# Optimization experiments

Measured on AMD Instinct MI355X. Metric: run time of the kernel, lower is better.

## Reference

```python
import jax, jax.numpy as jnp
import numpy as np

N_NODES = 100000
N_EDGES = 800000
IN_C = 128
HID = 256
N_GRAPHS = 64
N_CLASSES = 2
BN_EPS = 1e-5


def setup_inputs() -> dict:
    key = jax.random.key(0)
    ks = jax.random.split(key, 10)
    s1 = 1.0 / np.sqrt(IN_C)
    s2 = 1.0 / np.sqrt(HID)
    s3 = 1.0 / np.sqrt(HID // 2)
    return {
        "x": jax.random.normal(ks[0], (N_NODES, IN_C), jnp.float32),
        "edge_index": jax.random.randint(ks[1], (2, N_EDGES), 0, N_NODES, dtype=jnp.int32),
        "batch": jnp.sort(jax.random.randint(ks[2], (N_NODES,), 0, N_GRAPHS, dtype=jnp.int32)),
        "W1a": jax.random.normal(ks[3], (IN_C, HID), jnp.float32) * s1,
        "W1r": jax.random.normal(ks[4], (IN_C, HID), jnp.float32) * s1,
        "b1": jnp.zeros((HID,), jnp.float32),
        "bn_gamma": jnp.ones((HID,), jnp.float32),
        "bn_beta": jnp.zeros((HID,), jnp.float32),
        "bn_mean": jnp.zeros((HID,), jnp.float32),
        "bn_var": jnp.ones((HID,), jnp.float32),
        "W2a": jax.random.normal(ks[5], (HID, HID), jnp.float32) * s2,
        "W2r": jax.random.normal(ks[6], (HID, HID), jnp.float32) * s2,
        "b2": jnp.zeros((HID,), jnp.float32),
        "Wc1": jax.random.normal(ks[7], (HID, HID // 2), jnp.float32) * s2,
        "bc1": jnp.zeros((HID // 2,), jnp.float32),
        "Wc2": jax.random.normal(ks[8], (HID // 2, N_CLASSES), jnp.float32) * s3,
        "bc2": jnp.zeros((N_CLASSES,), jnp.float32),
    }


def _sage_conv(x, src, dst, Wa, Wr, b):
    # mean-aggregate neighbor features: messages flow src -> dst
    msgs = x[src]                                             # [E, C] gather
    summed = jax.ops.segment_sum(msgs, dst, num_segments=N_NODES)
    deg = jax.ops.segment_sum(jnp.ones((src.shape[0],), x.dtype), dst,
                              num_segments=N_NODES)
    agg = summed / jnp.maximum(deg, 1.0)[:, None]
    return agg @ Wa + x @ Wr + b                              # lin_l(agg) + lin_r(x)


def reference(x, edge_index, batch, W1a, W1r, b1, bn_gamma, bn_beta, bn_mean,
              bn_var, W2a, W2r, b2, Wc1, bc1, Wc2, bc2):
    src, dst = edge_index[0], edge_index[1]
    # layer 1: SAGEConv -> BatchNorm (eval, running stats) -> ReLU (dropout off)
    h = _sage_conv(x, src, dst, W1a, W1r, b1)
    h = (h - bn_mean) * jax.lax.rsqrt(bn_var + BN_EPS) * bn_gamma + bn_beta
    h = jax.nn.relu(h)
    # layer 2: SAGEConv (no BN/ReLU after last conv)
    h = _sage_conv(h, src, dst, W2a, W2r, b2)
    # global mean pool per graph
    pooled = jax.ops.segment_sum(h, batch, num_segments=N_GRAPHS)
    cnt = jax.ops.segment_sum(jnp.ones((N_NODES,), h.dtype), batch,
                              num_segments=N_GRAPHS)
    g = pooled / jnp.maximum(cnt, 1.0)[:, None]
    # classifier MLP + log_softmax
    g = jax.nn.relu(g @ Wc1 + bc1)
    logits = g @ Wc2 + bc2
    return jax.nn.log_softmax(logits, axis=-1)
```

## Files before the change

kernel.cpp:

```cpp
#include <hip/hip_runtime.h>
#include <math.h>

#define N_NODES 100000
#define IN_C 128
#define HID 256
#define N_GRAPHS 64
#define BN_EPS 1e-5f
#define CAP 32
#define NTILES (N_NODES / 16)
#define KSTEPS (N_NODES / 32)
#define POOL_KB 250

typedef unsigned int   uint32;
typedef unsigned short ushort16;
typedef __attribute__((ext_vector_type(8))) short bf16x8;
typedef __attribute__((ext_vector_type(4))) float f32x4;

__device__ __forceinline__ float bf_lo(uint32 u) { return __builtin_bit_cast(float, u << 16); }
__device__ __forceinline__ float bf_hi(uint32 u) { return __builtin_bit_cast(float, u & 0xffff0000u); }
__device__ __forceinline__ ushort16 f2bf(float f) {
    uint32 u = __builtin_bit_cast(uint32, f);
    return (ushort16)((u + 0x7fffu + ((u >> 16) & 1u)) >> 16);
}

__global__ __launch_bounds__(256) void k_cvt_x(const float* __restrict__ x,
                                               ushort16* __restrict__ xf,
                                               ushort16* __restrict__ xb) {
    int gid = blockIdx.x * blockDim.x + threadIdx.x;
    int lane = gid & 63;
    int ts = gid >> 6;
    int t = ts >> 2, s = ts & 3;
    int n = t * 16 + (lane & 15);
    int k0 = s * 32 + (lane >> 4) * 8;
    const float* xp = &x[(size_t)n * IN_C + k0];
    float4 a = *(const float4*)xp;
    float4 b = *(const float4*)(xp + 4);
    bf16x8 pk;
    pk[0] = (short)f2bf(a.x); pk[1] = (short)f2bf(a.y);
    pk[2] = (short)f2bf(a.z); pk[3] = (short)f2bf(a.w);
    pk[4] = (short)f2bf(b.x); pk[5] = (short)f2bf(b.y);
    pk[6] = (short)f2bf(b.z); pk[7] = (short)f2bf(b.w);
    *(bf16x8*)(xf + (size_t)gid * 8) = pk;
    *(bf16x8*)(xb + (size_t)n * IN_C + k0) = pk;
}

__global__ void k_prep_w(const float* __restrict__ W1r, const float* __restrict__ W1a,
                         ushort16* __restrict__ WThi, ushort16* __restrict__ WTlo) {
    int c = blockIdx.x;
    int k = threadIdx.x;
    float v = (k < 128) ? W1r[(size_t)k * 256 + c] : W1a[(size_t)(k - 128) * 256 + c];
    ushort16 h = f2bf(v);
    float vh = __builtin_bit_cast(float, ((uint32)h) << 16);
    ushort16 l = f2bf(v - vh);
    size_t idx = ((((size_t)(c >> 4) * 8 + (k >> 5)) * 64 + ((k >> 3) & 3) * 16 + (c & 15)) * 8) + (k & 7);
    WThi[idx] = h;
    WTlo[idx] = l;
}

__global__ void k_fill2(const int* __restrict__ dst, const int* __restrict__ srcv,
                        int* __restrict__ pos, int* __restrict__ col, int E) {
    int e = blockIdx.x * blockDim.x + threadIdx.x;
    if (e >= E) return;
    int d = dst[e];
    int slot = atomicAdd(&pos[d], 1);
    if (slot < CAP) col[(size_t)d * CAP + slot] = srcv[e];
}

__global__ __launch_bounds__(256) void k_cnt(const int* __restrict__ batch,
                                             float* __restrict__ cnt, int N) {
    __shared__ int h[64];
    int t = threadIdx.x;
    if (t < 64) h[t] = 0;
    __syncthreads();
    int n = blockIdx.x * 256 + t;
    if (n < N) atomicAdd(&h[batch[n]], 1);
    __syncthreads();
    if (t < 64 && h[t]) atomicAdd(&cnt[t], (float)h[t]);
}

__global__ __launch_bounds__(256) void k_cvt_c(const float* __restrict__ C,
                                               const int* __restrict__ batch,
                                               ushort16* __restrict__ Cb) {
    int gid = blockIdx.x * 256 + threadIdx.x;
    int l = gid & 63;
    int ktjt = gid >> 6;
    int jt = ktjt & 7;
    int kt = ktjt >> 3;
    int j = jt * 16 + (l & 15);
    int nb = kt * 32 + ((l >> 4) << 3);
    bf16x8 pk;
#pragma unroll
    for (int jj = 0; jj < 8; jj++) {
        int n = nb + jj;
        float v;
        if (j < 64) v = C[(size_t)n * 64 + j];
        else v = (batch[n] == (j - 64)) ? 1.0f : 0.0f;
        pk[jj] = (short)f2bf(v);
    }
    *(bf16x8*)(Cb + (size_t)gid * 8) = pk;
}

__global__ __launch_bounds__(256) void k_agg1(const uint32* __restrict__ xb2,
                                              const int* __restrict__ pos,
                                              const int* __restrict__ col,
                                              const int* __restrict__ batch,
                                              float* __restrict__ C,
                                              uint32* __restrict__ af32, int N) {
    int node = (int)((blockIdx.x * blockDim.x + threadIdx.x) >> 6);
    int lane = threadIdx.x & 63;
    if (node >= N) return;
    int deg = min(pos[node], CAP);
    int g = batch[node];
    float invw = 1.0f / (float)max(deg, 1);
    int sv = 0;
    if (lane < CAP) sv = col[(size_t)node * CAP + lane];
    if (lane < deg) atomicAdd(&C[(size_t)sv * 64 + g], invw);

    float ax = 0.f, ay = 0.f;
    int j = 0;
    for (; j + 8 <= deg; j += 8) {
        int s0 = __shfl(sv, j + 0), s1 = __shfl(sv, j + 1);
        int s2 = __shfl(sv, j + 2), s3 = __shfl(sv, j + 3);
        int s4 = __shfl(sv, j + 4), s5 = __shfl(sv, j + 5);
        int s6 = __shfl(sv, j + 6), s7 = __shfl(sv, j + 7);
        uint32 u0 = xb2[(size_t)s0 * 64 + lane];
        uint32 u1 = xb2[(size_t)s1 * 64 + lane];
        uint32 u2 = xb2[(size_t)s2 * 64 + lane];
        uint32 u3 = xb2[(size_t)s3 * 64 + lane];
        uint32 u4 = xb2[(size_t)s4 * 64 + lane];
        uint32 u5 = xb2[(size_t)s5 * 64 + lane];
        uint32 u6 = xb2[(size_t)s6 * 64 + lane];
        uint32 u7 = xb2[(size_t)s7 * 64 + lane];
        ax += ((bf_lo(u0) + bf_lo(u1)) + (bf_lo(u2) + bf_lo(u3))) +
              ((bf_lo(u4) + bf_lo(u5)) + (bf_lo(u6) + bf_lo(u7)));
        ay += ((bf_hi(u0) + bf_hi(u1)) + (bf_hi(u2) + bf_hi(u3))) +
              ((bf_hi(u4) + bf_hi(u5)) + (bf_hi(u6) + bf_hi(u7)));
    }
    for (; j < deg; j++) {
        int s = __shfl(sv, j);
        uint32 u = xb2[(size_t)s * 64 + lane];
        ax += bf_lo(u); ay += bf_hi(u);
    }
    uint32 p = (uint32)f2bf(ax * invw) | (((uint32)f2bf(ay * invw)) << 16);
    int k = 2 * lane;
    int ks = k >> 5, lg = (k >> 3) & 3, j2 = (k & 7) >> 1;
    int koff = (ks * 64 + lg * 16) * 4 + j2;
    af32[(size_t)(node >> 4) * 1024 + (node & 15) * 4 + koff] = p;
}

__global__ __launch_bounds__(256) void k_gemm1(
        const ushort16* __restrict__ xf, const ushort16* __restrict__ af,
        const ushort16* __restrict__ WThi, const ushort16* __restrict__ WTlo,
        const float* __restrict__ b1, const float* __restrict__ gamma,
        const float* __restrict__ beta, const float* __restrict__ mean,
        const float* __restrict__ var, ushort16* __restrict__ h1T, int N) {
    int n0 = blockIdx.x * 64;
    int w = threadIdx.x >> 6;
    int l = threadIdx.x & 63;
    int l15 = l & 15;
    int lg = l >> 4;
    int ocb = w * 64;
    int t0 = n0 >> 4;

    f32x4 acc[4][4];
#pragma unroll
    for (int i = 0; i < 4; i++)
#pragma unroll
        for (int j = 0; j < 4; j++) acc[i][j] = (f32x4)0.f;

    int tt[4];
#pragma unroll
    for (int nt = 0; nt < 4; nt++) tt[nt] = min(t0 + nt, NTILES - 1);

#pragma unroll
    for (int ks = 0; ks < 4; ks++) {
        bf16x8 wh[4], wl[4], bx[4];
#pragma unroll
        for (int ot = 0; ot < 4; ot++) {
            size_t fb = ((size_t)(w * 4 + ot) * 8 + ks) * 64 + l;
            wh[ot] = *(const bf16x8*)(WThi + fb * 8);
            wl[ot] = *(const bf16x8*)(WTlo + fb * 8);
        }
#pragma unroll
        for (int nt = 0; nt < 4; nt++)
            bx[nt] = *(const bf16x8*)(xf + (((size_t)tt[nt] * 4 + ks) * 64 + l) * 8);
#pragma unroll
        for (int ot = 0; ot < 4; ot++)
#pragma unroll
            for (int nt = 0; nt < 4; nt++) {
                acc[ot][nt] = __builtin_amdgcn_mfma_f32_16x16x32_bf16(wh[ot], bx[nt], acc[ot][nt], 0, 0, 0);
                acc[ot][nt] = __builtin_amdgcn_mfma_f32_16x16x32_bf16(wl[ot], bx[nt], acc[ot][nt], 0, 0, 0);
            }
    }
#pragma unroll
    for (int ks = 0; ks < 4; ks++) {
        bf16x8 wh[4], wl[4], bx[4];
#pragma unroll
        for (int ot = 0; ot < 4; ot++) {
            size_t fb = ((size_t)(w * 4 + ot) * 8 + 4 + ks) * 64 + l;
            wh[ot] = *(const bf16x8*)(WThi + fb * 8);
            wl[ot] = *(const bf16x8*)(WTlo + fb * 8);
        }
#pragma unroll
        for (int nt = 0; nt < 4; nt++)
            bx[nt] = *(const bf16x8*)(af + (((size_t)tt[nt] * 4 + ks) * 64 + l) * 8);
#pragma unroll
        for (int ot = 0; ot < 4; ot++)
#pragma unroll
            for (int nt = 0; nt < 4; nt++) {
                acc[ot][nt] = __builtin_amdgcn_mfma_f32_16x16x32_bf16(wh[ot], bx[nt], acc[ot][nt], 0, 0, 0);
                acc[ot][nt] = __builtin_amdgcn_mfma_f32_16x16x32_bf16(wl[ot], bx[nt], acc[ot][nt], 0, 0, 0);
            }
    }

#pragma unroll
    for (int ot = 0; ot < 4; ot++) {
        int c = ocb + ot * 16 + lg * 4;
        float4 gm = *(const float4*)&gamma[c];
        float4 bt = *(const float4*)&beta[c];
        float4 mn = *(const float4*)&mean[c];
        float4 vr = *(const float4*)&var[c];
        float4 bb = *(const float4*)&b1[c];
        float s0 = gm.x * rsqrtf(vr.x + BN_EPS);
        float s1 = gm.y * rsqrtf(vr.y + BN_EPS);
        float s2 = gm.z * rsqrtf(vr.z + BN_EPS);
        float s3 = gm.w * rsqrtf(vr.w + BN_EPS);
        float o0 = bt.x + (bb.x - mn.x) * s0;
        float o1 = bt.y + (bb.y - mn.y) * s1;
        float o2 = bt.z + (bb.z - mn.z) * s2;
        float o3 = bt.w + (bb.w - mn.w) * s3;
#pragma unroll
        for (int nt = 0; nt < 4; nt++) {
            int n = n0 + nt * 16 + l15;
            if (n < N) {
                f32x4 a = acc[ot][nt];
                h1T[(size_t)(c + 0) * N_NODES + n] = f2bf(fmaxf(a[0] * s0 + o0, 0.f));
                h1T[(size_t)(c + 1) * N_NODES + n] = f2bf(fmaxf(a[1] * s1 + o1, 0.f));
                h1T[(size_t)(c + 2) * N_NODES + n] = f2bf(fmaxf(a[2] * s2 + o2, 0.f));
                h1T[(size_t)(c + 3) * N_NODES + n] = f2bf(fmaxf(a[3] * s3 + o3, 0.f));
            }
        }
    }
}

__global__ __launch_bounds__(512) void k_pool(const ushort16* __restrict__ h1T,
                                              const ushort16* __restrict__ Cb,
                                              float* __restrict__ part) {
    int blk = blockIdx.x;
    int w = threadIdx.x >> 6;
    int l = threadIdx.x & 63;
    int l15 = l & 15, lg = l >> 4;
    int ks = (int)(((long)blk * KSTEPS) / POOL_KB);
    int ke = (int)(((long)(blk + 1) * KSTEPS) / POOL_KB);
    f32x4 acc[2][8];
#pragma unroll
    for (int i = 0; i < 2; i++)
#pragma unroll
        for (int j = 0; j < 8; j++) acc[i][j] = (f32x4)0.f;

    size_t arow0 = (size_t)(w * 32 + l15) * N_NODES + lg * 8;
    size_t arow1 = arow0 + (size_t)16 * N_NODES;
    for (int k = ks; k < ke; k++) {
        int n0 = k * 32;
        bf16x8 a0 = *(const bf16x8*)(h1T + arow0 + n0);
        bf16x8 a1 = *(const bf16x8*)(h1T + arow1 + n0);
        const ushort16* cb = Cb + ((size_t)k * 512 + l) * 8;
#pragma unroll
        for (int jt = 0; jt < 8; jt++) {
            bf16x8 b = *(const bf16x8*)(cb + (size_t)jt * 512);
            acc[0][jt] = __builtin_amdgcn_mfma_f32_16x16x32_bf16(a0, b, acc[0][jt], 0, 0, 0);
            acc[1][jt] = __builtin_amdgcn_mfma_f32_16x16x32_bf16(a1, b, acc[1][jt], 0, 0, 0);
        }
    }
    float* pb = part + (size_t)blk * 32768;
#pragma unroll
    for (int ci = 0; ci < 2; ci++)
#pragma unroll
        for (int jt = 0; jt < 8; jt++)
#pragma unroll
            for (int r = 0; r < 4; r++) {
                int c = w * 32 + ci * 16 + lg * 4 + r;
                int j = jt * 16 + l15;
                pb[c * 128 + j] = acc[ci][jt][r];
            }
}

__global__ __launch_bounds__(256) void k_red(const float* __restrict__ part,
                                             float* __restrict__ P1,
                                             float* __restrict__ P2) {
    __shared__ float sh[256];
    int b = blockIdx.x;
    int t = threadIdx.x;
    int idl = t & 127;
    int half = t >> 7;
    int id = b * 128 + idl;
    float s = 0.f;
    for (int kb = half; kb < POOL_KB; kb += 2)
        s += part[(size_t)kb * 32768 + id];
    sh[t] = s;
    __syncthreads();
    if (half == 0) {
        float v = sh[t] + sh[t + 128];
        int c = id >> 7, jj = id & 127;
        if (jj < 64) P2[jj * 256 + c] = v;
        else         P1[(jj - 64) * 256 + c] = v;
    }
}

__global__ __launch_bounds__(256) void k_classifier(
        const float* __restrict__ P1, const float* __restrict__ P2,
        const float* __restrict__ cnt,
        const float* __restrict__ W2a, const float* __restrict__ W2r,
        const float* __restrict__ b2,
        const float* __restrict__ Wc1, const float* __restrict__ bc1,
        const float* __restrict__ Wc2, const float* __restrict__ bc2,
        float* __restrict__ out) {
    __shared__ float p1s[256], p2s[256], g2[256], c1s[128], lg[2];
    int g = blockIdx.x, t = threadIdx.x;
    p1s[t] = P1[g * 256 + t];
    p2s[t] = P2[g * 256 + t];
    __syncthreads();
    float acc = 0.f;
    for (int k = 0; k < 256; k++)
        acc += p2s[k] * W2a[k * 256 + t] + p1s[k] * W2r[k * 256 + t];
    float c = cnt[g];
    float inv = 1.0f / fmaxf(c, 1.0f);
    g2[t] = (acc + c * b2[t]) * inv;
    __syncthreads();
    if (t < 128) {
        float a = bc1[t];
        for (int k = 0; k < 256; k++) a += g2[k] * Wc1[k * 128 + t];
        c1s[t] = fmaxf(a, 0.f);
    }
    __syncthreads();
    if (t < 2) {
        float a = bc2[t];
        for (int k = 0; k < 128; k++) a += c1s[k] * Wc2[k * 2 + t];
        lg[t] = a;
    }
    __syncthreads();
    if (t == 0) {
        float m = fmaxf(lg[0], lg[1]);
        float lse = m + logf(expf(lg[0] - m) + expf(lg[1] - m));
        out[g * 2 + 0] = lg[0] - lse;
        out[g * 2 + 1] = lg[1] - lse;
    }
}

extern "C" void kernel_launch(void* const* d_in, const int* in_sizes, int n_in,
                              void* d_out, int out_size, void* d_ws, size_t ws_size,
                              hipStream_t stream) {
    const float* x     = (const float*)d_in[0];
    const int*   edge  = (const int*)d_in[1];
    const int*   batch = (const int*)d_in[2];
    const float* W1a   = (const float*)d_in[3];
    const float* W1r   = (const float*)d_in[4];
    const float* b1    = (const float*)d_in[5];
    const float* gamma = (const float*)d_in[6];
    const float* beta  = (const float*)d_in[7];
    const float* mean  = (const float*)d_in[8];
    const float* var   = (const float*)d_in[9];
    const float* W2a   = (const float*)d_in[10];
    const float* W2r   = (const float*)d_in[11];
    const float* b2    = (const float*)d_in[12];
    const float* Wc1   = (const float*)d_in[13];
    const float* bc1   = (const float*)d_in[14];
    const float* Wc2   = (const float*)d_in[15];
    const float* bc2   = (const float*)d_in[16];
    float* out = (float*)d_out;

    const int N = N_NODES;
    const int E = in_sizes[1] / 2;
    const int* src = edge;
    const int* dst = edge + E;

    char* wsp = (char*)d_ws;
    auto alloc = [&](size_t bytes) {
        char* p = wsp;
        wsp += (bytes + 255) & ~(size_t)255;
        return p;
    };
    const size_t HALF = (size_t)N * 128 * 2;
    int*      pos    = (int*)alloc((size_t)N * 4);
    float*    cnt    = (float*)alloc(256 * 4);
    char*     zero_end = wsp;
    int*      col    = (int*)alloc((size_t)N * CAP * 4);
    float*    P1     = (float*)alloc((size_t)N_GRAPHS * 256 * 4);
    float*    P2     = (float*)alloc((size_t)N_GRAPHS * 256 * 4);
    char*     regA   = alloc(2 * HALF);
    ushort16* xb     = (ushort16*)regA;
    float*    C      = (float*)(regA + HALF);
    ushort16* h1T    = (ushort16*)regA;
    char*     regB   = alloc(2 * HALF);
    ushort16* xf     = (ushort16*)regB;
    ushort16* af     = (ushort16*)(regB + HALF);
    float*    part   = (float*)regB;
    ushort16* Cb     = (ushort16*)alloc((size_t)N * 128 * 2);
    ushort16* WThi   = (ushort16*)alloc((size_t)HID * HID * 2);
    ushort16* WTlo   = (ushort16*)alloc((size_t)HID * HID * 2);

    hipMemsetAsync(pos, 0, (size_t)(zero_end - (char*)pos), stream);
    hipMemsetAsync(C, 0, HALF, stream);

    k_cvt_x<<<N * IN_C / 8 / 256, 256, 0, stream>>>(x, xf, xb);
    k_prep_w<<<HID, HID, 0, stream>>>(W1r, W1a, WThi, WTlo);
    k_fill2<<<(E + 255) / 256, 256, 0, stream>>>(dst, src, pos, col, E);
    k_cnt<<<(N + 255) / 256, 256, 0, stream>>>(batch, cnt, N);
    k_agg1<<<(N + 3) / 4, 256, 0, stream>>>((const uint32*)xb, pos, col, batch, C,
                                            (uint32*)af, N);
    k_cvt_c<<<KSTEPS * 512 / 256, 256, 0, stream>>>(C, batch, Cb);
    k_gemm1<<<(N + 63) / 64, 256, 0, stream>>>(xf, af, WThi, WTlo, b1, gamma, beta,
                                               mean, var, h1T, N);
    k_pool<<<POOL_KB, 512, 0, stream>>>(h1T, Cb, part);
    k_red<<<256, 256, 0, stream>>>(part, P1, P2);
    k_classifier<<<N_GRAPHS, 256, 0, stream>>>(P1, P2, cnt, W2a, W2r, b2,
                                               Wc1, bc1, Wc2, bc2, out);
}
```

Before: 393.1 us.

## Process two nodes per wave in aggregation and transpose graph-weight scatter buffer

The first-layer aggregation now assigns each node to a half-wave of 32 lanes. Each lane loads 8 bytes (4 bf16 channels) per neighbor, and the neighbor loop uses masked 8-wide batches instead of a separate remainder loop. The per-graph weight scatter buffer is transposed to graph-major (graph x node), so k_cvt_c reads 8 consecutive nodes contiguously rather than strided by 64. These changes aim to raise memory-level parallelism, improve coalescing of the C conversion, and cut wasted lanes for low-degree nodes. In exchange, the masked loads fetch row 0 for inactive slots, and the atomics scatter across a wider address range.

```diff
diff --git a/kernel.cpp b/kernel.cpp
--- a/kernel.cpp
+++ b/kernel.cpp
@@ -78,7 +78,7 @@
     if (t < 64 && h[t]) atomicAdd(&cnt[t], (float)h[t]);
 }
 
-__global__ __launch_bounds__(256) void k_cvt_c(const float* __restrict__ C,
+__global__ __launch_bounds__(256) void k_cvt_c(const float* __restrict__ Cg,
                                                const int* __restrict__ batch,
                                                ushort16* __restrict__ Cb) {
     int gid = blockIdx.x * 256 + threadIdx.x;
@@ -89,13 +89,15 @@
     int j = jt * 16 + (l & 15);
     int nb = kt * 32 + ((l >> 4) << 3);
     bf16x8 pk;
-#pragma unroll
-    for (int jj = 0; jj < 8; jj++) {
-        int n = nb + jj;
-        float v;
-        if (j < 64) v = C[(size_t)n * 64 + j];
-        else v = (batch[n] == (j - 64)) ? 1.0f : 0.0f;
-        pk[jj] = (short)f2bf(v);
+    if (j < 64) {
+        const float* cp = &Cg[(size_t)j * N_NODES + nb];
+#pragma unroll
+        for (int jj = 0; jj < 8; jj++) pk[jj] = (short)f2bf(cp[jj]);
+    } else {
+        int jg = j - 64;
+#pragma unroll
+        for (int jj = 0; jj < 8; jj++)
+            pk[jj] = (short)f2bf((batch[nb + jj] == jg) ? 1.0f : 0.0f);
     }
     *(bf16x8*)(Cb + (size_t)gid * 8) = pk;
 }
@@ -104,48 +106,43 @@
                                               const int* __restrict__ pos,
                                               const int* __restrict__ col,
                                               const int* __restrict__ batch,
-                                              float* __restrict__ C,
+                                              float* __restrict__ Cg,
                                               uint32* __restrict__ af32, int N) {
-    int node = (int)((blockIdx.x * blockDim.x + threadIdx.x) >> 6);
+    int wid = (int)((blockIdx.x * blockDim.x + threadIdx.x) >> 6);
     int lane = threadIdx.x & 63;
+    int lh = lane & 31;
+    int node = wid * 2 + (lane >> 5);
     if (node >= N) return;
     int deg = min(pos[node], CAP);
     int g = batch[node];
     float invw = 1.0f / (float)max(deg, 1);
-    int sv = 0;
-    if (lane < CAP) sv = col[(size_t)node * CAP + lane];
-    if (lane < deg) atomicAdd(&C[(size_t)sv * 64 + g], invw);
-
-    float ax = 0.f, ay = 0.f;
-    int j = 0;
-    for (; j + 8 <= deg; j += 8) {
-        int s0 = __shfl(sv, j + 0), s1 = __shfl(sv, j + 1);
-        int s2 = __shfl(sv, j + 2), s3 = __shfl(sv, j + 3);
-        int s4 = __shfl(sv, j + 4), s5 = __shfl(sv, j + 5);
-        int s6 = __shfl(sv, j + 6), s7 = __shfl(sv, j + 7);
-        uint32 u0 = xb2[(size_t)s0 * 64 + lane];
-        uint32 u1 = xb2[(size_t)s1 * 64 + lane];
-        uint32 u2 = xb2[(size_t)s2 * 64 + lane];
-        uint32 u3 = xb2[(size_t)s3 * 64 + lane];
-        uint32 u4 = xb2[(size_t)s4 * 64 + lane];
-        uint32 u5 = xb2[(size_t)s5 * 64 + lane];
-        uint32 u6 = xb2[(size_t)s6 * 64 + lane];
-        uint32 u7 = xb2[(size_t)s7 * 64 + lane];
-        ax += ((bf_lo(u0) + bf_lo(u1)) + (bf_lo(u2) + bf_lo(u3))) +
-              ((bf_lo(u4) + bf_lo(u5)) + (bf_lo(u6) + bf_lo(u7)));
-        ay += ((bf_hi(u0) + bf_hi(u1)) + (bf_hi(u2) + bf_hi(u3))) +
-              ((bf_hi(u4) + bf_hi(u5)) + (bf_hi(u6) + bf_hi(u7)));
-    }
-    for (; j < deg; j++) {
-        int s = __shfl(sv, j);
-        uint32 u = xb2[(size_t)s * 64 + lane];
-        ax += bf_lo(u); ay += bf_hi(u);
-    }
-    uint32 p = (uint32)f2bf(ax * invw) | (((uint32)f2bf(ay * invw)) << 16);
-    int k = 2 * lane;
-    int ks = k >> 5, lg = (k >> 3) & 3, j2 = (k & 7) >> 1;
-    int koff = (ks * 64 + lg * 16) * 4 + j2;
-    af32[(size_t)(node >> 4) * 1024 + (node & 15) * 4 + koff] = p;
+    int sv = col[(size_t)node * CAP + lh];
+    if (lh < deg) atomicAdd(&Cg[(size_t)g * N_NODES + sv], invw);
+
+    float a0 = 0.f, a1 = 0.f, a2 = 0.f, a3 = 0.f;
+    for (int j = 0; j < deg; j += 8) {
+        uint2 u[8];
+        float m[8];
+#pragma unroll
+        for (int q = 0; q < 8; q++) {
+            int act = (j + q) < deg;
+            int s = __shfl(sv, j + q, 32);
+            s = act ? s : 0;
+            m[q] = act ? 1.f : 0.f;
+            u[q] = *(const uint2*)&xb2[(size_t)s * 64 + lh * 2];
+        }
+#pragma unroll
+        for (int q = 0; q < 8; q++) {
+            a0 += m[q] * bf_lo(u[q].x); a1 += m[q] * bf_hi(u[q].x);
+            a2 += m[q] * bf_lo(u[q].y); a3 += m[q] * bf_hi(u[q].y);
+        }
+    }
+    uint2 o;
+    o.x = (uint32)f2bf(a0 * invw) | (((uint32)f2bf(a1 * invw)) << 16);
+    o.y = (uint32)f2bf(a2 * invw) | (((uint32)f2bf(a3 * invw)) << 16);
+    int ks = lh >> 3, lg = (lh >> 1) & 3, j2 = (lh & 1) * 2;
+    size_t idx = (size_t)(node >> 4) * 1024 + (size_t)(ks * 64 + lg * 16 + (node & 15)) * 4 + j2;
+    *(uint2*)&af32[idx] = o;
 }
 
 __global__ __launch_bounds__(256) void k_gemm1(
@@ -389,7 +386,7 @@
     float*    P2     = (float*)alloc((size_t)N_GRAPHS * 256 * 4);
     char*     regA   = alloc(2 * HALF);
     ushort16* xb     = (ushort16*)regA;
-    float*    C      = (float*)(regA + HALF);
+    float*    Cg     = (float*)(regA + HALF);
     ushort16* h1T    = (ushort16*)regA;
     char*     regB   = alloc(2 * HALF);
     ushort16* xf     = (ushort16*)regB;
@@ -400,15 +397,15 @@
     ushort16* WTlo   = (ushort16*)alloc((size_t)HID * HID * 2);
 
     hipMemsetAsync(pos, 0, (size_t)(zero_end - (char*)pos), stream);
-    hipMemsetAsync(C, 0, HALF, stream);
+    hipMemsetAsync(Cg, 0, HALF, stream);
 
     k_cvt_x<<<N * IN_C / 8 / 256, 256, 0, stream>>>(x, xf, xb);
     k_prep_w<<<HID, HID, 0, stream>>>(W1r, W1a, WThi, WTlo);
     k_fill2<<<(E + 255) / 256, 256, 0, stream>>>(dst, src, pos, col, E);
     k_cnt<<<(N + 255) / 256, 256, 0, stream>>>(batch, cnt, N);
-    k_agg1<<<(N + 3) / 4, 256, 0, stream>>>((const uint32*)xb, pos, col, batch, C,
+    k_agg1<<<(N + 7) / 8, 256, 0, stream>>>((const uint32*)xb, pos, col, batch, Cg,
                                             (uint32*)af, N);
-    k_cvt_c<<<KSTEPS * 512 / 256, 256, 0, stream>>>(C, batch, Cb);
+    k_cvt_c<<<KSTEPS * 512 / 256, 256, 0, stream>>>(Cg, batch, Cb);
     k_gemm1<<<(N + 63) / 64, 256, 0, stream>>>(xf, af, WThi, WTlo, b1, gamma, beta,
                                                mean, var, h1T, N);
     k_pool<<<POOL_KB, 512, 0, stream>>>(h1T, Cb, part);
```

Result: faster. 378.0 us (-3.8%).
